# Optimization experiments

Measured on AMD Instinct MI355X. Metric: run time of the kernel, lower is better.

## Reference

```python
import jax, jax.numpy as jnp
import numpy as np

N = 50000        # nodes
E = 800000       # edges (avg degree 16)
HID = 96         # hidden_channels
HEADS = 4        # heads passed to SRGATConv
D = HID // HEADS # per-head dim
R = 38           # num_relations
NEG_SLOPE = 0.2  # LeakyReLU slope for attention logits


def setup_inputs() -> dict:
    key = jax.random.key(0)
    ks = jax.random.split(key, 9)
    x = jax.random.normal(ks[0], (N, HID), jnp.float32)
    edge_index = jax.random.randint(ks[1], (2, E), 0, N, dtype=jnp.int32)
    edge_type = jax.random.randint(ks[2], (E,), 0, R, dtype=jnp.int32)
    s = 1.0 / np.sqrt(HID)
    W = jax.random.normal(ks[3], (HID, HID), jnp.float32) * s          # node projection
    rel_emb = jax.random.normal(ks[4], (R, HID), jnp.float32) * s      # relation embeddings
    att_src = jax.random.normal(ks[5], (HEADS, D), jnp.float32) * 0.1  # attention vectors
    att_dst = jax.random.normal(ks[6], (HEADS, D), jnp.float32) * 0.1
    att_rel = jax.random.normal(ks[7], (HEADS, D), jnp.float32) * 0.1
    bias = jnp.zeros((HID,), jnp.float32)
    return {"x": x, "edge_index": edge_index, "edge_type": edge_type,
            "W": W, "rel_emb": rel_emb, "att_src": att_src,
            "att_dst": att_dst, "att_rel": att_rel, "bias": bias}


def reference(x, edge_index, edge_type, W, rel_emb, att_src, att_dst, att_rel, bias):
    # SRGATConv: relation-aware multi-head graph attention, then GELU wrapper.
    n = x.shape[0]
    src, dst = edge_index[0], edge_index[1]
    h = (x @ W).reshape(n, HEADS, D)                    # [N,H,D]
    r = rel_emb[edge_type].reshape(-1, HEADS, D)        # [E,H,D] gathered relation feats
    h_src = h[src]                                      # [E,H,D] irregular gather
    h_dst = h[dst]
    # attention logits per edge/head
    logits = ((h_src * att_src).sum(-1)
              + (h_dst * att_dst).sum(-1)
              + (r * att_rel).sum(-1))                  # [E,H]
    logits = jax.nn.leaky_relu(logits, NEG_SLOPE)
    # segment softmax over incoming edges of each destination node
    lmax = jax.ops.segment_max(logits, dst, num_segments=n)   # [N,H]
    e = jnp.exp(logits - lmax[dst])
    denom = jax.ops.segment_sum(e, dst, num_segments=n)       # [N,H]
    alpha = e / denom[dst]                                    # [E,H]
    # weighted message scatter
    msg = alpha[:, :, None] * (h_src + r)                     # [E,H,D]
    out = jax.ops.segment_sum(msg, dst, num_segments=n).reshape(n, HID) + bias
    out = jax.nn.gelu(out)
    return out, alpha
```

## Files before the change

kernel.cpp:

```cpp
#include <hip/hip_runtime.h>
#include <hip/hip_fp16.h>
#include <math.h>

#define HIDC 96
#define HEADS 4
#define RMAX 40
#define BINSZ 64
#define BINB 6
#define BINCAP 1344
#define TILE 2048
#define SRCB 18
#define SRCM ((1 << SRCB) - 1)
#define ETB 6
#define NBMAX 1024

typedef unsigned u32x2 __attribute__((ext_vector_type(2)));

__device__ __forceinline__ __half2 u2h2(unsigned u) {
    return *reinterpret_cast<__half2*>(&u);
}
__device__ __forceinline__ unsigned h22u(__half2 h) {
    return *reinterpret_cast<unsigned*>(&h);
}

__global__ __launch_bounds__(192) void gemm96(const float* __restrict__ x,
                                              const float* __restrict__ W,
                                              __half* __restrict__ h16,
                                              int* __restrict__ bincnt,
                                              int4* __restrict__ csrtail,
                                              int n, int nbins) {
    for (int i = blockIdx.x * 192 + threadIdx.x; i < nbins; i += gridDim.x * 192)
        bincnt[i] = 0;
    if (blockIdx.x == 0 && threadIdx.x < 16)
        csrtail[threadIdx.x] = make_int4(0, 0, 0, 0);

    __shared__ float Ws[HIDC * HIDC];
    __shared__ float xs[32 * HIDC];
    for (int i = threadIdx.x; i < HIDC * HIDC / 4; i += 192)
        reinterpret_cast<float4*>(Ws)[i] = reinterpret_cast<const float4*>(W)[i];
    int c4 = threadIdx.x % 24;
    int r0 = (threadIdx.x / 24) * 4;
    const float4* xs4 = reinterpret_cast<const float4*>(xs);
    const float4* Ws4 = reinterpret_cast<const float4*>(Ws);
    uint2* h8 = reinterpret_cast<uint2*>(h16);
    int numTiles = (n + 31) >> 5;
    for (int tile = blockIdx.x; tile < numTiles; tile += gridDim.x) {
        int row0 = tile << 5;
        int rows = min(32, n - row0);
        __syncthreads();
        for (int i = threadIdx.x; i < rows * 24; i += 192)
            reinterpret_cast<float4*>(xs)[i] =
                reinterpret_cast<const float4*>(x + (size_t)row0 * HIDC)[i];
        __syncthreads();
        float4 acc[4];
#pragma unroll
        for (int i = 0; i < 4; ++i) acc[i] = make_float4(0.f, 0.f, 0.f, 0.f);
#pragma unroll 4
        for (int k4 = 0; k4 < 24; ++k4) {
            float4 xv[4], wv[4];
#pragma unroll
            for (int i = 0; i < 4; ++i) xv[i] = xs4[(r0 + i) * 24 + k4];
#pragma unroll
            for (int j = 0; j < 4; ++j) wv[j] = Ws4[(k4 * 4 + j) * 24 + c4];
#pragma unroll
            for (int i = 0; i < 4; ++i) {
                const float xi[4] = {xv[i].x, xv[i].y, xv[i].z, xv[i].w};
#pragma unroll
                for (int j = 0; j < 4; ++j) {
                    acc[i].x = fmaf(xi[j], wv[j].x, acc[i].x);
                    acc[i].y = fmaf(xi[j], wv[j].y, acc[i].y);
                    acc[i].z = fmaf(xi[j], wv[j].z, acc[i].z);
                    acc[i].w = fmaf(xi[j], wv[j].w, acc[i].w);
                }
            }
        }
#pragma unroll
        for (int i = 0; i < 4; ++i)
            if (r0 + i < rows) {
                __half2 lo = __floats2half2_rn(acc[i].x, acc[i].y);
                __half2 hi = __floats2half2_rn(acc[i].z, acc[i].w);
                uint2 pk;
                pk.x = h22u(lo);
                pk.y = h22u(hi);
                h8[(size_t)(row0 + r0 + i) * 24 + c4] = pk;
            }
    }
}

__global__ __launch_bounds__(256) void node_dots(
    const __half* __restrict__ h16,
    const float* __restrict__ att_src, const float* __restrict__ att_dst,
    const float* __restrict__ rel, const float* __restrict__ att_rel,
    float4* __restrict__ ps, float* __restrict__ pdi,
    float4* __restrict__ pr, int n, int R_) {
    if (blockIdx.x == gridDim.x - 1) {
        int t = threadIdx.x;
        if (t < R_) {
            const float4* rp = reinterpret_cast<const float4*>(rel + (size_t)t * HIDC);
            const float4* ar = reinterpret_cast<const float4*>(att_rel);
            float acc[HEADS] = {0, 0, 0, 0};
#pragma unroll
            for (int c = 0; c < 24; ++c) {
                float4 v = rp[c], a = ar[c];
                acc[c / 6] += v.x * a.x + v.y * a.y + v.z * a.z + v.w * a.w;
            }
            pr[t] = make_float4(acc[0], acc[1], acc[2], acc[3]);
        }
        return;
    }
    int i = blockIdx.x * blockDim.x + threadIdx.x;
    if (i >= n) return;
    const uint2* hp = reinterpret_cast<const uint2*>(h16 + (size_t)i * HIDC);
    const float4* as = reinterpret_cast<const float4*>(att_src);
    const float4* ad = reinterpret_cast<const float4*>(att_dst);
    float accs[HEADS] = {0, 0, 0, 0}, accd[HEADS] = {0, 0, 0, 0};
#pragma unroll
    for (int c = 0; c < 24; ++c) {
        uint2 hv = hp[c];
        float2 f0 = __half22float2(u2h2(hv.x));
        float2 f1 = __half22float2(u2h2(hv.y));
        float4 a = as[c], d = ad[c];
        int hh = c / 6;
        accs[hh] += f0.x * a.x + f0.y * a.y + f1.x * a.z + f1.y * a.w;
        accd[hh] += f0.x * d.x + f0.y * d.y + f1.x * d.z + f1.y * d.w;
    }
    ps[i] = make_float4(accs[0], accs[1], accs[2], accs[3]);
    *reinterpret_cast<float4*>(pdi + (size_t)i * 8) =
        make_float4(accd[0], accd[1], accd[2], accd[3]);
}

__device__ __forceinline__ float4 ev4(float4 a, float4 b, float4 c) {
    float l0 = a.x + b.x + c.x, l1 = a.y + b.y + c.y;
    float l2 = a.z + b.z + c.z, l3 = a.w + b.w + c.w;
    l0 = l0 >= 0.f ? l0 : 0.2f * l0;
    l1 = l1 >= 0.f ? l1 : 0.2f * l1;
    l2 = l2 >= 0.f ? l2 : 0.2f * l2;
    l3 = l3 >= 0.f ? l3 : 0.2f * l3;
    return make_float4(__expf(l0), __expf(l1), __expf(l2), __expf(l3));
}

__device__ __forceinline__ float gelu_f(float v) {
    float u = 0.7978845608028654f * (v + 0.044715f * v * v * v);
    u = fminf(fmaxf(u, -15.f), 15.f);
    float t = __expf(2.f * u);
    return 0.5f * v * (1.f + (t - 1.f) / (t + 1.f));
}

__global__ __launch_bounds__(256) void bin_edges(
    const int* __restrict__ src, const int* __restrict__ dst,
    const int* __restrict__ et,
    int* __restrict__ bincnt, int2* __restrict__ binwords,
    int E_, int nbins) {
    __shared__ int hist[NBMAX];
    __shared__ int base[NBMAX];
    int e0 = blockIdx.x * TILE;
    for (int i = threadIdx.x; i < nbins; i += 256) hist[i] = 0;
    __syncthreads();
    int mybin[8], myrank[8], myword[8];
#pragma unroll
    for (int u = 0; u < 8; ++u) {
        int e = e0 + u * 256 + threadIdx.x;
        mybin[u] = -1;
        if (e < E_) {
            int d = dst[e];
            int b = d >> BINB;
            myword[u] = src[e] | (et[e] << SRCB) | ((d & (BINSZ - 1)) << (SRCB + ETB));
            mybin[u] = b;
            myrank[u] = atomicAdd(&hist[b], 1);
        }
    }
    __syncthreads();
    for (int i = threadIdx.x; i < nbins; i += 256)
        base[i] = hist[i] > 0 ? atomicAdd(&bincnt[i], hist[i]) : 0;
    __syncthreads();
#pragma unroll
    for (int u = 0; u < 8; ++u) {
        if (mybin[u] >= 0) {
            int pos = base[mybin[u]] + myrank[u];
            if (pos < BINCAP)
                binwords[(size_t)mybin[u] * BINCAP + pos] =
                    make_int2(myword[u], e0 + u * 256 + threadIdx.x);
        }
    }
}

__global__ __launch_bounds__(256) void bin_sort(
    const int* __restrict__ bincnt, const int2* __restrict__ binwords,
    const float4* __restrict__ ps, const float* __restrict__ pdi,
    const float4* __restrict__ prg,
    int4* __restrict__ csr, int* __restrict__ noff, int* __restrict__ ncnt,
    int n, int R_) {
    __shared__ int cnts[BINSZ];
    __shared__ int scanb[BINSZ];
    __shared__ int nbase[BINSZ];
    __shared__ float4 pdl[BINSZ];
    __shared__ float4 prl[RMAX];
    int bin = blockIdx.x;
    int node0 = bin * BINSZ;
    int total = min(bincnt[bin], BINCAP);

    for (int i = threadIdx.x; i < BINSZ; i += 256) {
        cnts[i] = 0;
        int nd = node0 + i;
        pdl[i] = (nd < n) ? *reinterpret_cast<const float4*>(pdi + (size_t)nd * 8)
                          : make_float4(0.f, 0.f, 0.f, 0.f);
    }
    for (int i = threadIdx.x; i < R_; i += 256) prl[i] = prg[i];
    __syncthreads();

    int2 w[6];
    int rk[6];
#pragma unroll
    for (int u = 0; u < 6; ++u) {
        int k = u * 256 + threadIdx.x;
        rk[u] = -1;
        if (k < total) {
            w[u] = binwords[(size_t)bin * BINCAP + k];
            int dl = (w[u].x >> (SRCB + ETB)) & (BINSZ - 1);
            rk[u] = atomicAdd(&cnts[dl], 1);
        }
    }
    __syncthreads();

    if (threadIdx.x < BINSZ) scanb[threadIdx.x] = (cnts[threadIdx.x] + 3) & ~3;
    __syncthreads();
    for (int s = 1; s < BINSZ; s <<= 1) {
        int v = 0;
        if (threadIdx.x < BINSZ && threadIdx.x >= s) v = scanb[threadIdx.x - s];
        __syncthreads();
        if (threadIdx.x < BINSZ) scanb[threadIdx.x] += v;
        __syncthreads();
    }
    if (threadIdx.x < BINSZ) {
        int cnt = cnts[threadIdx.x];
        int cntP = (cnt + 3) & ~3;
        int nb = scanb[threadIdx.x] - cntP;
        nbase[threadIdx.x] = nb;
        int nd = node0 + threadIdx.x;
        if (nd < n) {
            noff[nd] = bin * BINCAP + nb;
            ncnt[nd] = cnt;
        }
        int4 z = make_int4(0, 0, 0, 0);
        for (int i = cnt; i < cntP; ++i)
            csr[(size_t)bin * BINCAP + nb + i] = z;
    }
    {
        int gt = scanb[BINSZ - 1];
        if (threadIdx.x < 12) {
            int p = gt + threadIdx.x;
            if (p < BINCAP)
                csr[(size_t)bin * BINCAP + p] = make_int4(0, 0, 0, 0);
        }
    }
    __syncthreads();

#pragma unroll
    for (int u = 0; u < 6; ++u) {
        if (rk[u] >= 0) {
            int s = w[u].x & SRCM;
            int t = (w[u].x >> SRCB) & ((1 << ETB) - 1);
            int dl = (w[u].x >> (SRCB + ETB)) & (BINSZ - 1);
            unsigned e = (unsigned)w[u].y;
            float4 v = ev4(ps[s], pdl[dl], prl[t]);
            int4 pk;
            pk.x = (int)((unsigned)(s * (HIDC * 2)) | ((e & 0xFFu) << 24));
            pk.y = (int)((unsigned)(t * (HIDC * 2)) | ((e >> 8) << 13));
            pk.z = (int)h22u(__floats2half2_rn(v.x, v.y));
            pk.w = (int)h22u(__floats2half2_rn(v.z, v.w));
            csr[(size_t)bin * BINCAP + nbase[dl] + rk[u]] = pk;
        }
    }
}

__global__ __launch_bounds__(256) void node_agg(
    const __half* __restrict__ h16, const float* __restrict__ rel,
    const int4* __restrict__ csr, const int* __restrict__ noff,
    const int* __restrict__ ncnt,
    const float* __restrict__ bias,
    float* __restrict__ out, float4* __restrict__ alpha, int n, int R_) {
    __shared__ uint2 relh[RMAX * HIDC / 4];
    for (int i = threadIdx.x; i < R_ * 24; i += 256) {
        float4 v = reinterpret_cast<const float4*>(rel)[i];
        uint2 pk;
        pk.x = h22u(__floats2half2_rn(v.x, v.y));
        pk.y = h22u(__floats2half2_rn(v.z, v.w));
        relh[i] = pk;
    }
    __syncthreads();

    int lane = threadIdx.x & 31;
    if (lane >= 24) return;
    const int j = lane;
    const int j4 = 4 * j;
    const int hh = j / 6;
    const unsigned joff = (unsigned)(j << 3);
    const float4 bv = *reinterpret_cast<const float4*>(bias + j4);
    const char* h16c = reinterpret_cast<const char*>(h16);
    const char* relc = reinterpret_cast<const char*>(relh);
    const unsigned esel = (unsigned)(2 * hh) | ((unsigned)(2 * hh + 1) << 8);

    int hw0 = (blockIdx.x * blockDim.x + threadIdx.x) >> 5;
    int nHW = (gridDim.x * blockDim.x) >> 5;

    for (int hw = hw0; hw < n; hw += nHW) {
        int cnt = ncnt[hw];
        const int4* sp0 = csr + noff[hw];
        const int4* sp = sp0;
        float a0 = 0.f, a1 = 0.f, a2 = 0.f, a3 = 0.f;
        float dsum = 0.f;

        if (cnt > 0) {
            int cntP = (cnt + 3) & ~3;
            int4 pc[4];
#pragma unroll
            for (int u = 0; u < 4; ++u) pc[u] = sp[u];
            sp += 4;

            for (int k = 0; k < cntP; k += 4, sp += 4) {
                uint2 hv[4], rv[4];
#pragma unroll
                for (int u = 0; u < 4; ++u)
                    hv[u] = *reinterpret_cast<const uint2*>(
                        h16c + ((unsigned)pc[u].x & 0x00FFFFFFu) + joff);
#pragma unroll
                for (int u = 0; u < 4; ++u)
                    rv[u] = *reinterpret_cast<const uint2*>(
                        relc + ((unsigned)pc[u].y & 0x1FFFu) + joff);
                int4 pn[4];
#pragma unroll
                for (int u = 0; u < 4; ++u) pn[u] = sp[u];
#pragma unroll
                for (int u = 0; u < 4; ++u) {
                    unsigned e32 = __builtin_amdgcn_perm(
                        (unsigned)pc[u].w, (unsigned)pc[u].z, esel);
                    dsum += __half2float(__low2half(u2h2(e32)));
                    unsigned s01 = h22u(__hadd2(u2h2(hv[u].x), u2h2(rv[u].x)));
                    unsigned s23 = h22u(__hadd2(u2h2(hv[u].y), u2h2(rv[u].y)));
                    asm("v_fma_mix_f32 %0, %1, %2, %0 op_sel:[0,0,0] op_sel_hi:[1,1,0]"
                        : "+v"(a0) : "v"(s01), "v"(e32));
                    asm("v_fma_mix_f32 %0, %1, %2, %0 op_sel:[1,0,0] op_sel_hi:[1,1,0]"
                        : "+v"(a1) : "v"(s01), "v"(e32));
                    asm("v_fma_mix_f32 %0, %1, %2, %0 op_sel:[0,0,0] op_sel_hi:[1,1,0]"
                        : "+v"(a2) : "v"(s23), "v"(e32));
                    asm("v_fma_mix_f32 %0, %1, %2, %0 op_sel:[1,0,0] op_sel_hi:[1,1,0]"
                        : "+v"(a3) : "v"(s23), "v"(e32));
                }
#pragma unroll
                for (int u = 0; u < 4; ++u) pc[u] = pn[u];
            }
        }
        float inv = dsum > 0.f ? 1.f / dsum : 0.f;
        float4 o;
        o.x = gelu_f(a0 * inv + bv.x);
        o.y = gelu_f(a1 * inv + bv.y);
        o.z = gelu_f(a2 * inv + bv.z);
        o.w = gelu_f(a3 * inv + bv.w);
        *reinterpret_cast<float4*>(out + (size_t)hw * HIDC + j4) = o;

        if (cnt > 0) {
            float iv0 = __shfl(inv, 0, 32);
            float iv1 = __shfl(inv, 6, 32);
            float iv2 = __shfl(inv, 12, 32);
            float iv3 = __shfl(inv, 18, 32);
            for (int k = j; k < cnt; k += 24) {
                int4 pk = sp0[k];
                unsigned e_id = ((unsigned)pk.x >> 24) | (((unsigned)pk.y >> 13) << 8);
                float2 f01 = __half22float2(u2h2((unsigned)pk.z));
                float2 f23 = __half22float2(u2h2((unsigned)pk.w));
                alpha[e_id] = make_float4(f01.x * iv0, f01.y * iv1,
                                          f23.x * iv2, f23.y * iv3);
            }
        }
    }
}

extern "C" void kernel_launch(void* const* d_in, const int* in_sizes, int n_in,
                              void* d_out, int out_size, void* d_ws, size_t ws_size,
                              hipStream_t stream) {
    const float* x       = (const float*)d_in[0];
    const int*   eidx    = (const int*)d_in[1];
    const int*   etype   = (const int*)d_in[2];
    const float* W       = (const float*)d_in[3];
    const float* rel     = (const float*)d_in[4];
    const float* att_src = (const float*)d_in[5];
    const float* att_dst = (const float*)d_in[6];
    const float* att_rel = (const float*)d_in[7];
    const float* bias    = (const float*)d_in[8];

    int N_ = in_sizes[0] / HIDC;
    int E_ = in_sizes[1] / 2;
    int R_ = in_sizes[4] / HIDC;
    const int* src  = eidx;
    const int* dstp = eidx + E_;
    int nbins = (N_ + BINSZ - 1) / BINSZ;

    char* ws = (char*)d_ws;
    __half* h16      = (__half*)ws; ws += (size_t)N_ * HIDC * 2;
    float4* ps       = (float4*)ws; ws += (size_t)N_ * 16;
    float*  pdi      = (float*)ws;  ws += (size_t)N_ * 32;
    float4* pr       = (float4*)ws; ws += 1024;
    int*    bincnt   = (int*)ws;    ws += (size_t)((nbins + 3) & ~3) * 4;
    int*    noff     = (int*)ws;    ws += (size_t)((N_ + 3) & ~3) * 4;
    int*    ncnt     = (int*)ws;    ws += (size_t)((N_ + 3) & ~3) * 4;
    int2*   binwords = (int2*)ws;   ws += (size_t)nbins * BINCAP * 8;
    int4*   csr      = (int4*)ws;   ws += (size_t)nbins * BINCAP * 16 + 256;

    float*  outv  = (float*)d_out;
    float4* alpha = (float4*)(outv + (size_t)N_ * HIDC);

    gemm96<<<(N_ + 31) / 32, 192, 0, stream>>>(
        x, W, h16, bincnt, csr + (size_t)nbins * BINCAP, N_, nbins);

    node_dots<<<(N_ + 255) / 256 + 1, 256, 0, stream>>>(
        h16, att_src, att_dst, rel, att_rel, ps, pdi, pr, N_, R_);

    bin_edges<<<(E_ + TILE - 1) / TILE, 256, 0, stream>>>(
        src, dstp, etype, bincnt, binwords, E_, nbins);

    bin_sort<<<nbins, 256, 0, stream>>>(
        bincnt, binwords, ps, pdi, pr, csr, noff, ncnt, N_, R_);

    node_agg<<<(N_ + 15) / 16, 256, 0, stream>>>(
        h16, rel, csr, noff, ncnt, bias, outv, alpha, N_, R_);
}
```

Before: 192.6 us.

## Use MFMA fp16 matrix cores for projection GEMM and prefetch source dots

New measurement: 177.4 us. 1.09x faster.

```diff
diff --git a/kernel.cpp b/kernel.cpp
--- a/kernel.cpp
+++ b/kernel.cpp
@@ -15,6 +15,8 @@
 #define NBMAX 1024
 
 typedef unsigned u32x2 __attribute__((ext_vector_type(2)));
+typedef _Float16 f16x4 __attribute__((ext_vector_type(4)));
+typedef float f32x4 __attribute__((ext_vector_type(4)));
 
 __device__ __forceinline__ __half2 u2h2(unsigned u) {
     return *reinterpret_cast<__half2*>(&u);
@@ -23,68 +25,63 @@
     return *reinterpret_cast<unsigned*>(&h);
 }
 
-__global__ __launch_bounds__(192) void gemm96(const float* __restrict__ x,
+__global__ __launch_bounds__(256) void gemm96(const float* __restrict__ x,
                                               const float* __restrict__ W,
                                               __half* __restrict__ h16,
                                               int* __restrict__ bincnt,
                                               int4* __restrict__ csrtail,
                                               int n, int nbins) {
-    for (int i = blockIdx.x * 192 + threadIdx.x; i < nbins; i += gridDim.x * 192)
+    for (int i = blockIdx.x * 256 + threadIdx.x; i < nbins; i += gridDim.x * 256)
         bincnt[i] = 0;
     if (blockIdx.x == 0 && threadIdx.x < 16)
         csrtail[threadIdx.x] = make_int4(0, 0, 0, 0);
 
-    __shared__ float Ws[HIDC * HIDC];
-    __shared__ float xs[32 * HIDC];
-    for (int i = threadIdx.x; i < HIDC * HIDC / 4; i += 192)
-        reinterpret_cast<float4*>(Ws)[i] = reinterpret_cast<const float4*>(W)[i];
-    int c4 = threadIdx.x % 24;
-    int r0 = (threadIdx.x / 24) * 4;
-    const float4* xs4 = reinterpret_cast<const float4*>(xs);
-    const float4* Ws4 = reinterpret_cast<const float4*>(Ws);
-    uint2* h8 = reinterpret_cast<uint2*>(h16);
-    int numTiles = (n + 31) >> 5;
-    for (int tile = blockIdx.x; tile < numTiles; tile += gridDim.x) {
-        int row0 = tile << 5;
-        int rows = min(32, n - row0);
-        __syncthreads();
-        for (int i = threadIdx.x; i < rows * 24; i += 192)
-            reinterpret_cast<float4*>(xs)[i] =
-                reinterpret_cast<const float4*>(x + (size_t)row0 * HIDC)[i];
-        __syncthreads();
-        float4 acc[4];
-#pragma unroll
-        for (int i = 0; i < 4; ++i) acc[i] = make_float4(0.f, 0.f, 0.f, 0.f);
-#pragma unroll 4
-        for (int k4 = 0; k4 < 24; ++k4) {
-            float4 xv[4], wv[4];
-#pragma unroll
-            for (int i = 0; i < 4; ++i) xv[i] = xs4[(r0 + i) * 24 + k4];
-#pragma unroll
-            for (int j = 0; j < 4; ++j) wv[j] = Ws4[(k4 * 4 + j) * 24 + c4];
-#pragma unroll
-            for (int i = 0; i < 4; ++i) {
-                const float xi[4] = {xv[i].x, xv[i].y, xv[i].z, xv[i].w};
-#pragma unroll
-                for (int j = 0; j < 4; ++j) {
-                    acc[i].x = fmaf(xi[j], wv[j].x, acc[i].x);
-                    acc[i].y = fmaf(xi[j], wv[j].y, acc[i].y);
-                    acc[i].z = fmaf(xi[j], wv[j].z, acc[i].z);
-                    acc[i].w = fmaf(xi[j], wv[j].w, acc[i].w);
-                }
-            }
-        }
-#pragma unroll
-        for (int i = 0; i < 4; ++i)
-            if (r0 + i < rows) {
-                __half2 lo = __floats2half2_rn(acc[i].x, acc[i].y);
-                __half2 hi = __floats2half2_rn(acc[i].z, acc[i].w);
-                uint2 pk;
-                pk.x = h22u(lo);
-                pk.y = h22u(hi);
-                h8[(size_t)(row0 + r0 + i) * 24 + c4] = pk;
-            }
-    }
+    const int lane = threadIdx.x & 63;
+    const int wave = threadIdx.x >> 6;
+    const int lo16 = lane & 15;
+    const int grp = lane >> 4;
+
+    f16x4 bf[6][6];
+#pragma unroll
+    for (int kf = 0; kf < 6; ++kf)
+#pragma unroll
+        for (int nt = 0; nt < 6; ++nt) {
+            f16x4 b;
+#pragma unroll
+            for (int j = 0; j < 4; ++j)
+                b[j] = (_Float16)W[(kf * 16 + grp * 4 + j) * HIDC + nt * 16 + lo16];
+            bf[kf][nt] = b;
+        }
+
+    int row0 = blockIdx.x * 64 + wave * 16;
+    if (row0 >= n) return;
+    int r = row0 + lo16;
+    const float4* xr = reinterpret_cast<const float4*>(
+        x + (size_t)min(r, n - 1) * HIDC);
+
+    f32x4 c[6];
+#pragma unroll
+    for (int nt = 0; nt < 6; ++nt) c[nt] = (f32x4){0.f, 0.f, 0.f, 0.f};
+
+#pragma unroll
+    for (int kf = 0; kf < 6; ++kf) {
+        float4 av = xr[kf * 4 + grp];
+        f16x4 af;
+        af[0] = (_Float16)av.x; af[1] = (_Float16)av.y;
+        af[2] = (_Float16)av.z; af[3] = (_Float16)av.w;
+#pragma unroll
+        for (int nt = 0; nt < 6; ++nt)
+            c[nt] = __builtin_amdgcn_mfma_f32_16x16x16f16(af, bf[kf][nt], c[nt], 0, 0, 0);
+    }
+
+#pragma unroll
+    for (int nt = 0; nt < 6; ++nt)
+#pragma unroll
+        for (int i = 0; i < 4; ++i) {
+            int rr = row0 + grp * 4 + i;
+            if (rr < n)
+                h16[(size_t)rr * HIDC + nt * 16 + lo16] = (__half)c[nt][i];
+        }
 }
 
 __global__ __launch_bounds__(256) void node_dots(
@@ -210,12 +207,14 @@
 
     int2 w[6];
     int rk[6];
+    float4 psv[6];
 #pragma unroll
     for (int u = 0; u < 6; ++u) {
         int k = u * 256 + threadIdx.x;
         rk[u] = -1;
         if (k < total) {
             w[u] = binwords[(size_t)bin * BINCAP + k];
+            psv[u] = ps[w[u].x & SRCM];
             int dl = (w[u].x >> (SRCB + ETB)) & (BINSZ - 1);
             rk[u] = atomicAdd(&cnts[dl], 1);
         }
@@ -262,7 +261,7 @@
             int t = (w[u].x >> SRCB) & ((1 << ETB) - 1);
             int dl = (w[u].x >> (SRCB + ETB)) & (BINSZ - 1);
             unsigned e = (unsigned)w[u].y;
-            float4 v = ev4(ps[s], pdl[dl], prl[t]);
+            float4 v = ev4(psv[u], pdl[dl], prl[t]);
             int4 pk;
             pk.x = (int)((unsigned)(s * (HIDC * 2)) | ((e & 0xFFu) << 24));
             pk.y = (int)((unsigned)(t * (HIDC * 2)) | ((e >> 8) << 13));
@@ -409,7 +408,7 @@
     float*  outv  = (float*)d_out;
     float4* alpha = (float4*)(outv + (size_t)N_ * HIDC);
 
-    gemm96<<<(N_ + 31) / 32, 192, 0, stream>>>(
+    gemm96<<<(N_ + 63) / 64, 256, 0, stream>>>(
         x, W, h16, bincnt, csr + (size_t)nbins * BINCAP, N_, nbins);
 
     node_dots<<<(N_ + 255) / 256 + 1, 256, 0, stream>>>(
```
